# Kernel optimization log

Hardware: AMD Instinct MI355X
Metric: run time of the kernel (lower is better)

The kernel has to match this reference:

```python
import jax, jax.numpy as jnp
import numpy as np

B, T, D, H = 4, 2048, 1024, 16
HD = D // H  # 64


def setup_inputs() -> dict:
    key = jax.random.key(0)
    ks = jax.random.split(key, 5)
    x = jax.random.normal(ks[0], (B, T, D), dtype=jnp.float32)
    # per-head projection weights, stacked over heads: [H, D, HD]
    # (torch Linear weight is [out,in]=[HD,D]; we store transposed so q = x @ Wq[h])
    Wq = jax.random.normal(ks[1], (H, D, HD), dtype=jnp.float32) * 0.02
    Wk = jax.random.normal(ks[2], (H, D, HD), dtype=jnp.float32) * 0.02
    Wv = jax.random.normal(ks[3], (H, D, HD), dtype=jnp.float32) * 0.02
    # output projection, torch convention: out = concat @ Wo.T, Wo: [D, D]
    Wo = jax.random.normal(ks[4], (D, D), dtype=jnp.float32) * 0.02
    return {"x": x, "Wq": Wq, "Wk": Wk, "Wv": Wv, "Wo": Wo}


def reference(x, Wq, Wk, Wv, Wo):
    # batched per-head projections: [B,T,D] x [H,D,K] -> [B,H,T,K]
    q = jnp.einsum('btd,hdk->bhtk', x, Wq)
    k = jnp.einsum('btd,hdk->bhtk', x, Wk)
    v = jnp.einsum('btd,hdk->bhtk', x, Wv)
    scale = 1.0 / jnp.sqrt(jnp.asarray(q.shape[-1], q.dtype))
    scores = jnp.einsum('bhtk,bhsk->bhts', q, k) * scale  # [B,H,T,T]
    attn = jax.nn.softmax(scores, axis=-1)
    out = jnp.einsum('bhts,bhsk->bhtk', attn, v)  # [B,H,T,K]
    # concat heads (head-major order == torch.cat over head list)
    concat = out.transpose(0, 2, 1, 3).reshape(x.shape[0], x.shape[1], -1)  # [B,T,D]
    return jnp.einsum('bte,de->btd', concat, Wo)
```

## Files before the change

kernel.cpp:

```cpp
#include <hip/hip_runtime.h>
#include <math.h>

#define B_ 4
#define T_ 2048
#define D_ 1024
#define H_ 16
#define HD_ 64
#define BT_ (B_ * T_)

typedef __attribute__((ext_vector_type(8))) short bf16x8;
typedef __attribute__((ext_vector_type(8))) _Float16 f16x8;
typedef __attribute__((ext_vector_type(4))) float f32x4;
typedef __attribute__((ext_vector_type(4))) unsigned int u32x4;
typedef unsigned short u16;
typedef unsigned int u32;

__device__ __forceinline__ u16 f2bf(float f) {
  u32 u = __float_as_uint(f);
  u32 r = (u + 0x7FFFu + ((u >> 16) & 1u)) >> 16;
  return (u16)r;
}
__device__ __forceinline__ float bf2f(u16 b) {
  return __uint_as_float(((u32)b) << 16);
}
__device__ __forceinline__ u16 f2h(float f) {
  _Float16 h = (_Float16)f;
  return __builtin_bit_cast(u16, h);
}
__device__ __forceinline__ float h2f(u16 b) {
  return (float)__builtin_bit_cast(_Float16, b);
}
__device__ __forceinline__ u32 cvtpk(float lo, float hi) {
  u32 r;
  asm("v_cvt_pk_bf16_f32 %0, %1, %2" : "=v"(r) : "v"(lo), "v"(hi));
  return r;
}
__device__ __forceinline__ void gload16(const u16* g, u16* l) {
  __builtin_amdgcn_global_load_lds(
      (const __attribute__((address_space(1))) unsigned int*)g,
      (__attribute__((address_space(3))) unsigned int*)l, 16, 0, 0);
}

__global__ __launch_bounds__(256) void convert_f16(
    const float* __restrict__ src, u16* __restrict__ dst, int n4) {
  int i = blockIdx.x * 256 + threadIdx.x;
  const int stride = gridDim.x * 256;
  for (; i < n4; i += stride) {
    float4 v = ((const float4*)src)[i];
    ((ushort4*)dst)[i] = make_ushort4(f2h(v.x), f2h(v.y), f2h(v.z), f2h(v.w));
  }
}

__global__ __launch_bounds__(256) void convert_wt(
    const float* __restrict__ Wq, const float* __restrict__ Wk,
    const float* __restrict__ Wv, u16* __restrict__ wtf) {
  const int d0 = blockIdx.x * 64;
  const int h = blockIdx.y;
  const int z = blockIdx.z;
  const float* W = (z == 0 ? Wq : (z == 1 ? Wk : Wv)) + (size_t)h * D_ * HD_;
  __shared__ float Tl[64][65];
  const int tid = threadIdx.x;
  const int r = tid >> 2;
  const int c0 = (tid & 3) * 16;
#pragma unroll
  for (int j = 0; j < 16; j += 4) {
    float4 v = *(const float4*)(W + (size_t)(d0 + r) * HD_ + c0 + j);
    Tl[c0 + j + 0][r] = v.x; Tl[c0 + j + 1][r] = v.y;
    Tl[c0 + j + 2][r] = v.z; Tl[c0 + j + 3][r] = v.w;
  }
  __syncthreads();
  u16* oh = wtf + (((size_t)z * H_ + h) * HD_ + r) * D_ + d0 + c0;
#pragma unroll
  for (int j = 0; j < 16; j += 4) {
    *(ushort4*)(oh + j) =
        make_ushort4(f2h(Tl[r][c0 + j]), f2h(Tl[r][c0 + j + 1]),
                     f2h(Tl[r][c0 + j + 2]), f2h(Tl[r][c0 + j + 3]));
  }
}

__global__ __launch_bounds__(256, 2) void qkv_mfma(
    const u16* __restrict__ xf, const u16* __restrict__ wtf,
    u16* __restrict__ Qb, u16* __restrict__ Kb, u16* __restrict__ Vtb) {
  const int m0 = blockIdx.x * 128;
  const int h = blockIdx.y;
  __shared__ __align__(16) u16 Xs[128 * 64];
  __shared__ __align__(16) u16 Ws[3 * 64 * 64];
  const int tid = threadIdx.x;
  const int lane = tid & 63, wave = tid >> 6;
  const int q = lane & 15, g = lane >> 4;

  f32x4 acc[3][2][4];
#pragma unroll
  for (int z = 0; z < 3; ++z)
#pragma unroll
    for (int mt = 0; mt < 2; ++mt)
#pragma unroll
      for (int nt = 0; nt < 4; ++nt)
#pragma unroll
        for (int r = 0; r < 4; ++r) acc[z][mt][nt][r] = 0.f;

  for (int k0 = 0; k0 < D_; k0 += 64) {
#pragma unroll
    for (int i = 0; i < 4; ++i) {
      const int l = wave * 4 + i;
      const int chunk = l * 64 + lane;
      const int row = chunk >> 3, sb = chunk & 7;
      const int so = (sb ^ (row & 7)) * 8;
      gload16(xf + (size_t)(m0 + row) * D_ + k0 + so, &Xs[l * 512]);
    }
#pragma unroll
    for (int z = 0; z < 3; ++z)
#pragma unroll
      for (int i = 0; i < 2; ++i) {
        const int l = wave * 2 + i;
        const int chunk = l * 64 + lane;
        const int row = chunk >> 3, sb = chunk & 7;
        const int so = (sb ^ (row & 7)) * 8;
        gload16(wtf + (((size_t)z * H_ + h) * HD_ + row) * D_ + k0 + so,
                &Ws[z * 4096 + l * 512]);
      }
    __syncthreads();
#pragma unroll
    for (int ks = 0; ks < 2; ++ks) {
      f16x8 ax[2];
#pragma unroll
      for (int mt = 0; mt < 2; ++mt) {
        const int arow = wave * 32 + mt * 16 + q;
        const int ab = arow * 128 + (((g + ks * 4) ^ (arow & 7)) * 16);
        ax[mt] = *(const f16x8*)((const char*)Xs + ab);
      }
#pragma unroll
      for (int z = 0; z < 3; ++z)
#pragma unroll
        for (int nt = 0; nt < 4; ++nt) {
          const int brow = nt * 16 + q;
          const int bb =
              z * 8192 + brow * 128 + (((g + ks * 4) ^ (brow & 7)) * 16);
          f16x8 bw = *(const f16x8*)((const char*)Ws + bb);
#pragma unroll
          for (int mt = 0; mt < 2; ++mt)
            acc[z][mt][nt] = __builtin_amdgcn_mfma_f32_16x16x32_f16(
                ax[mt], bw, acc[z][mt][nt], 0, 0, 0);
        }
    }
    __syncthreads();
  }

  const int b = m0 / T_;
  const int trow0 = m0 % T_;
  const float QSC = 0.125f * 1.44269504f;
  u16* Qd = Qb + (size_t)(b * H_ + h) * T_ * HD_;
  u16* Kd = Kb + (size_t)(b * H_ + h) * T_ * HD_;
  u16* Vd = Vtb + (size_t)(b * H_ + h) * HD_ * T_;
#pragma unroll
  for (int mt = 0; mt < 2; ++mt) {
    const int t_base = trow0 + wave * 32 + mt * 16 + g * 4;
#pragma unroll
    for (int nt = 0; nt < 4; ++nt) {
      const int d = nt * 16 + q;
#pragma unroll
      for (int r = 0; r < 4; ++r) {
        Qd[(size_t)(t_base + r) * HD_ + d] = f2bf(acc[0][mt][nt][r] * QSC);
        Kd[(size_t)(t_base + r) * HD_ + d] = f2bf(acc[1][mt][nt][r]);
      }
      ushort4 v = make_ushort4(f2bf(acc[2][mt][nt][0]), f2bf(acc[2][mt][nt][1]),
                               f2bf(acc[2][mt][nt][2]), f2bf(acc[2][mt][nt][3]));
      *(ushort4*)(Vd + (size_t)d * T_ + t_base) = v;
    }
  }
}

__global__ __launch_bounds__(256) void attn_mfma(
    const u16* __restrict__ Qb, const u16* __restrict__ Kb,
    const u16* __restrict__ Vtb, u16* __restrict__ ch, u16* __restrict__ cl) {
  const int q0 = blockIdx.x * 64;
  const int h = blockIdx.y;
  const int b = blockIdx.z;
  __shared__ __align__(16) u16 Ks[64 * 64];
  __shared__ __align__(16) u16 Vs[80 * 64];
  const int tid = threadIdx.x;
  const int lane = tid & 63, wave = tid >> 6;
  const int q = lane & 15, g = lane >> 4;

  const u16* Qg = Qb + ((size_t)(b * H_ + h) * T_ + q0 + wave * 16 + q) * HD_;
  const u16* Kg = Kb + (size_t)(b * H_ + h) * T_ * HD_;
  const u16* Vg = Vtb + (size_t)(b * H_ + h) * HD_ * T_;

  {
    u16* vext = &Vs[64 * 64];
    for (int i = tid; i < 16 * 64; i += 256) vext[i] = (i < 64) ? 0x3F80 : 0;
  }

  const bf16x8 qf0 = *(const bf16x8*)(Qg + g * 8);
  const bf16x8 qf1 = *(const bf16x8*)(Qg + 32 + g * 8);

  f32x4 ot[4], ot4;
#pragma unroll
  for (int t = 0; t < 4; ++t)
#pragma unroll
    for (int r = 0; r < 4; ++r) ot[t][r] = 0.f;
#pragma unroll
  for (int r = 0; r < 4; ++r) ot4[r] = 0.f;
  float m_run = -INFINITY;

  for (int kt = 0; kt < T_; kt += 64) {
#pragma unroll
    for (int c = 0; c < 2; ++c) {
      const int cc = wave * 2 + c;
      const int slot = cc * 64 + lane;
      const int row = slot >> 3, sb = slot & 7;
      const int so = (sb ^ (row & 7)) * 8;
      gload16(Kg + (size_t)(kt + row) * HD_ + so, &Ks[cc * 512]);
      gload16(Vg + (size_t)row * T_ + kt + so, &Vs[cc * 512]);
    }
    __syncthreads();

    f32x4 st[4];
#pragma unroll
    for (int t = 0; t < 4; ++t)
#pragma unroll
      for (int r = 0; r < 4; ++r) st[t][r] = 0.f;
#pragma unroll
    for (int ks = 0; ks < 2; ++ks) {
      const bf16x8 qf = ks ? qf1 : qf0;
#pragma unroll
      for (int t = 0; t < 4; ++t) {
        const int row = t * 16 + q;
        const int byte = row * 128 + (((g + ks * 4) ^ (row & 7)) * 16);
        bf16x8 kf = *(const bf16x8*)((const char*)Ks + byte);
        st[t] = __builtin_amdgcn_mfma_f32_16x16x32_bf16(kf, qf, st[t], 0, 0, 0);
      }
    }

    float mx = st[0][0];
#pragma unroll
    for (int t = 0; t < 4; ++t)
#pragma unroll
      for (int r = 0; r < 4; ++r) mx = fmaxf(mx, st[t][r]);
    mx = fmaxf(mx, __shfl_xor(mx, 16));
    mx = fmaxf(mx, __shfl_xor(mx, 32));
    if (!__all(mx <= m_run + 8.f)) {
      const float mnew = fmaxf(m_run, mx);
      const float al = __builtin_amdgcn_exp2f(m_run - mnew);
      m_run = mnew;
#pragma unroll
      for (int t = 0; t < 4; ++t)
#pragma unroll
        for (int r = 0; r < 4; ++r) ot[t][r] *= al;
#pragma unroll
      for (int r = 0; r < 4; ++r) ot4[r] *= al;
    }
    u32 pk[4][2];
#pragma unroll
    for (int t = 0; t < 4; ++t) {
      const float p0 = __builtin_amdgcn_exp2f(st[t][0] - m_run);
      const float p1 = __builtin_amdgcn_exp2f(st[t][1] - m_run);
      const float p2 = __builtin_amdgcn_exp2f(st[t][2] - m_run);
      const float p3 = __builtin_amdgcn_exp2f(st[t][3] - m_run);
      pk[t][0] = cvtpk(p0, p1);
      pk[t][1] = cvtpk(p2, p3);
    }

#pragma unroll
    for (int ks = 0; ks < 2; ++ks) {
      u32 bw[4];
#pragma unroll
      for (int w = 0; w < 4; ++w) {
        const int srcl = ((2 * g + (w >> 1)) & 3) * 16 + q;
        const u32 lo = (u32)__shfl((int)pk[ks * 2][w & 1], srcl);
        const u32 hi2 = (u32)__shfl((int)pk[ks * 2 + 1][w & 1], srcl);
        bw[w] = (g >> 1) ? hi2 : lo;
      }
      u32x4 tmp = {bw[0], bw[1], bw[2], bw[3]};
      bf16x8 pf = __builtin_bit_cast(bf16x8, tmp);
#pragma unroll
      for (int t = 0; t < 4; ++t) {
        const int row = t * 16 + q;
        const int byte = row * 128 + (((g + ks * 4) ^ (row & 7)) * 16);
        bf16x8 vf = *(const bf16x8*)((const char*)Vs + byte);
        ot[t] = __builtin_amdgcn_mfma_f32_16x16x32_bf16(vf, pf, ot[t], 0, 0, 0);
      }
      {
        const int row = 64 + q;
        const int byte = row * 128 + (((g + ks * 4) ^ (row & 7)) * 16);
        bf16x8 vf = *(const bf16x8*)((const char*)Vs + byte);
        ot4 = __builtin_amdgcn_mfma_f32_16x16x32_bf16(vf, pf, ot4, 0, 0, 0);
      }
    }
    __syncthreads();
  }

  const float lsum = __shfl(ot4[0], q);
  const float inv = 1.f / lsum;
  const size_t rowbase = (size_t)(b * T_ + q0 + wave * 16 + q) * D_ + h * HD_;
#pragma unroll
  for (int t = 0; t < 4; ++t) {
    float v0 = ot[t][0] * inv, v1 = ot[t][1] * inv;
    float v2 = ot[t][2] * inv, v3 = ot[t][3] * inv;
    ushort4 vh = make_ushort4(f2h(v0), f2h(v1), f2h(v2), f2h(v3));
    ushort4 vl =
        make_ushort4(f2h(v0 - h2f(vh.x)), f2h(v1 - h2f(vh.y)),
                     f2h(v2 - h2f(vh.z)), f2h(v3 - h2f(vh.w)));
    *(ushort4*)(ch + rowbase + t * 16 + g * 4) = vh;
    *(ushort4*)(cl + rowbase + t * 16 + g * 4) = vl;
  }
}

__global__ __launch_bounds__(256, 2) void oproj_mfma(
    const u16* __restrict__ ch_g, const u16* __restrict__ cl_g,
    const u16* __restrict__ wo_g, float* __restrict__ out) {
  const int m0 = blockIdx.x * 128;
  const int n0 = blockIdx.y * 128;
  __shared__ __align__(16) u16 Ah[128 * 64];
  __shared__ __align__(16) u16 Al[128 * 64];
  __shared__ __align__(16) u16 Bs[128 * 64];
  const int tid = threadIdx.x;
  const int lane = tid & 63, wave = tid >> 6;
  const int q = lane & 15, g = lane >> 4;

  f32x4 acc[2][8];
#pragma unroll
  for (int mt = 0; mt < 2; ++mt)
#pragma unroll
    for (int nt = 0; nt < 8; ++nt)
#pragma unroll
      for (int r = 0; r < 4; ++r) acc[mt][nt][r] = 0.f;

  for (int k0 = 0; k0 < D_; k0 += 64) {
#pragma unroll
    for (int i = 0; i < 4; ++i) {
      const int l = wave * 4 + i;
      const int chunk = l * 64 + lane;
      const int row = chunk >> 3, sb = chunk & 7;
      const int so = (sb ^ (row & 7)) * 8;
      const size_t ga = (size_t)(m0 + row) * D_ + k0 + so;
      const size_t gb = (size_t)(n0 + row) * D_ + k0 + so;
      gload16(ch_g + ga, &Ah[l * 512]);
      gload16(cl_g + ga, &Al[l * 512]);
      gload16(wo_g + gb, &Bs[l * 512]);
    }
    __syncthreads();
#pragma unroll
    for (int ks = 0; ks < 2; ++ks) {
      f16x8 axh[2], axl[2];
#pragma unroll
      for (int mt = 0; mt < 2; ++mt) {
        const int arow = wave * 32 + mt * 16 + q;
        const int ab = arow * 128 + (((g + ks * 4) ^ (arow & 7)) * 16);
        axh[mt] = *(const f16x8*)((const char*)Ah + ab);
        axl[mt] = *(const f16x8*)((const char*)Al + ab);
      }
#pragma unroll
      for (int nt = 0; nt < 8; ++nt) {
        const int brow = nt * 16 + q;
        const int bb = brow * 128 + (((g + ks * 4) ^ (brow & 7)) * 16);
        f16x8 bw = *(const f16x8*)((const char*)Bs + bb);
#pragma unroll
        for (int mt = 0; mt < 2; ++mt) {
          acc[mt][nt] = __builtin_amdgcn_mfma_f32_16x16x32_f16(
              axh[mt], bw, acc[mt][nt], 0, 0, 0);
          acc[mt][nt] = __builtin_amdgcn_mfma_f32_16x16x32_f16(
              axl[mt], bw, acc[mt][nt], 0, 0, 0);
        }
      }
    }
    __syncthreads();
  }

#pragma unroll
  for (int mt = 0; mt < 2; ++mt) {
    const int mrow = m0 + wave * 32 + mt * 16 + g * 4;
#pragma unroll
    for (int nt = 0; nt < 8; ++nt)
#pragma unroll
      for (int r = 0; r < 4; ++r)
        out[(size_t)(mrow + r) * D_ + n0 + nt * 16 + q] = acc[mt][nt][r];
  }
}

extern "C" void kernel_launch(void* const* d_in, const int* in_sizes, int n_in,
                              void* d_out, int out_size, void* d_ws,
                              size_t ws_size, hipStream_t stream) {
  const float* x = (const float*)d_in[0];
  const float* Wq = (const float*)d_in[1];
  const float* Wk = (const float*)d_in[2];
  const float* Wv = (const float*)d_in[3];
  const float* Wo = (const float*)d_in[4];
  float* out = (float*)d_out;

  u16* ws16 = (u16*)d_ws;
  u16* xf   = ws16;
  u16* wtf  = ws16 + 8388608;
  u16* wof  = ws16 + 11534336;
  u16* Qb   = ws16 + 12582912;
  u16* Kb   = ws16 + 20971520;
  u16* Vtb  = ws16 + 29360128;
  u16* c_lo = ws16 + 37748736;
  u16* c_hi = xf;

  convert_f16<<<2048, 256, 0, stream>>>(x, xf, BT_ * D_ / 4);
  convert_f16<<<1024, 256, 0, stream>>>(Wo, wof, D_ * D_ / 4);
  convert_wt<<<dim3(D_ / 64, H_, 3), 256, 0, stream>>>(Wq, Wk, Wv, wtf);
  qkv_mfma<<<dim3(BT_ / 128, H_), 256, 0, stream>>>(xf, wtf, Qb, Kb, Vtb);
  attn_mfma<<<dim3(T_ / 64, H_, B_), 256, 0, stream>>>(Qb, Kb, Vtb, c_hi, c_lo);
  oproj_mfma<<<dim3(BT_ / 128, D_ / 128), 256, 0, stream>>>(c_hi, c_lo, wof,
                                                            out);
}
```

Measured before the change: 319.0 us.

## Load K/V fragments straight from global into registers, dropping LDS staging

The attention kernel no longer stages K and V tiles through shared memory with block-wide barriers. Each wave now reads its K and V MFMA fragments directly from global memory into registers. The softmax row-sum is computed with a constant all-ones bf16 operand instead of a padded ones row in LDS, which also removes a lane shuffle at the end. This removes the LDS round trip and the two __syncthreads per tile. In exchange, every wave in a block re-fetches the same K/V data, which quadruples L2 and global load traffic, and the loads lose the cooperative coalesced pattern.

```diff
diff --git a/kernel.cpp b/kernel.cpp
--- a/kernel.cpp
+++ b/kernel.cpp
@@ -176,24 +176,21 @@
   const int q0 = blockIdx.x * 64;
   const int h = blockIdx.y;
   const int b = blockIdx.z;
-  __shared__ __align__(16) u16 Ks[64 * 64];
-  __shared__ __align__(16) u16 Vs[80 * 64];
   const int tid = threadIdx.x;
   const int lane = tid & 63, wave = tid >> 6;
   const int q = lane & 15, g = lane >> 4;
 
   const u16* Qg = Qb + ((size_t)(b * H_ + h) * T_ + q0 + wave * 16 + q) * HD_;
-  const u16* Kg = Kb + (size_t)(b * H_ + h) * T_ * HD_;
-  const u16* Vg = Vtb + (size_t)(b * H_ + h) * HD_ * T_;
-
-  {
-    u16* vext = &Vs[64 * 64];
-    for (int i = tid; i < 16 * 64; i += 256) vext[i] = (i < 64) ? 0x3F80 : 0;
-  }
+  const u16* kbase = Kb + (size_t)(b * H_ + h) * T_ * HD_ + (size_t)q * HD_ + g * 8;
+  const u16* vbase = Vtb + (size_t)(b * H_ + h) * HD_ * T_ + (size_t)q * T_ + g * 8;
 
   const bf16x8 qf0 = *(const bf16x8*)(Qg + g * 8);
   const bf16x8 qf1 = *(const bf16x8*)(Qg + 32 + g * 8);
 
+  bf16x8 ones;
+#pragma unroll
+  for (int j = 0; j < 8; ++j) ones[j] = (short)0x3F80;
+
   f32x4 ot[4], ot4;
 #pragma unroll
   for (int t = 0; t < 4; ++t)
@@ -204,16 +201,13 @@
   float m_run = -INFINITY;
 
   for (int kt = 0; kt < T_; kt += 64) {
-#pragma unroll
-    for (int c = 0; c < 2; ++c) {
-      const int cc = wave * 2 + c;
-      const int slot = cc * 64 + lane;
-      const int row = slot >> 3, sb = slot & 7;
-      const int so = (sb ^ (row & 7)) * 8;
-      gload16(Kg + (size_t)(kt + row) * HD_ + so, &Ks[cc * 512]);
-      gload16(Vg + (size_t)row * T_ + kt + so, &Vs[cc * 512]);
-    }
-    __syncthreads();
+    bf16x8 kf[2][4];
+#pragma unroll
+    for (int ks = 0; ks < 2; ++ks)
+#pragma unroll
+      for (int t = 0; t < 4; ++t)
+        kf[ks][t] =
+            *(const bf16x8*)(kbase + (size_t)(kt + t * 16) * HD_ + ks * 32);
 
     f32x4 st[4];
 #pragma unroll
@@ -224,12 +218,9 @@
     for (int ks = 0; ks < 2; ++ks) {
       const bf16x8 qf = ks ? qf1 : qf0;
 #pragma unroll
-      for (int t = 0; t < 4; ++t) {
-        const int row = t * 16 + q;
-        const int byte = row * 128 + (((g + ks * 4) ^ (row & 7)) * 16);
-        bf16x8 kf = *(const bf16x8*)((const char*)Ks + byte);
-        st[t] = __builtin_amdgcn_mfma_f32_16x16x32_bf16(kf, qf, st[t], 0, 0, 0);
-      }
+      for (int t = 0; t < 4; ++t)
+        st[t] =
+            __builtin_amdgcn_mfma_f32_16x16x32_bf16(kf[ks][t], qf, st[t], 0, 0, 0);
     }
 
     float mx = st[0][0];
@@ -275,22 +266,15 @@
       bf16x8 pf = __builtin_bit_cast(bf16x8, tmp);
 #pragma unroll
       for (int t = 0; t < 4; ++t) {
-        const int row = t * 16 + q;
-        const int byte = row * 128 + (((g + ks * 4) ^ (row & 7)) * 16);
-        bf16x8 vf = *(const bf16x8*)((const char*)Vs + byte);
+        bf16x8 vf =
+            *(const bf16x8*)(vbase + (size_t)(t * 16) * T_ + kt + ks * 32);
         ot[t] = __builtin_amdgcn_mfma_f32_16x16x32_bf16(vf, pf, ot[t], 0, 0, 0);
       }
-      {
-        const int row = 64 + q;
-        const int byte = row * 128 + (((g + ks * 4) ^ (row & 7)) * 16);
-        bf16x8 vf = *(const bf16x8*)((const char*)Vs + byte);
-        ot4 = __builtin_amdgcn_mfma_f32_16x16x32_bf16(vf, pf, ot4, 0, 0, 0);
-      }
-    }
-    __syncthreads();
-  }
-
-  const float lsum = __shfl(ot4[0], q);
+      ot4 = __builtin_amdgcn_mfma_f32_16x16x32_bf16(ones, pf, ot4, 0, 0, 0);
+    }
+  }
+
+  const float lsum = ot4[0];
   const float inv = 1.f / lsum;
   const size_t rowbase = (size_t)(b * T_ + q0 + wave * 16 + q) * D_ + h * HD_;
 #pragma unroll
```

Result: slower. 631.9 us (+98.1%).
